# Performance work log

Measured on AMD Instinct MI355X. Metric: run time of the kernel, lower is better.

The kernel has to match this reference:

```python
import jax, jax.numpy as jnp
import numpy as np
from jax import lax

STRIDE = 2
PADDING = 2
KERNEL = 5


def _conv_transpose3d(x, weight, bias):
    # weight: [C_in, C_out, kd, kh, kw] (PyTorch ConvTranspose3d layout)
    # Equivalent dense conv: flip kernel spatially, swap in/out channels,
    # lhs_dilation=stride, symmetric padding = dilation*(k-1) - padding.
    w_t = jnp.flip(weight, axis=(2, 3, 4)).transpose(1, 0, 2, 3, 4)  # [C_out, C_in, k,k,k]
    pad = KERNEL - 1 - PADDING  # = 2
    y = lax.conv_general_dilated(
        x, w_t,
        window_strides=(1, 1, 1),
        padding=[(pad, pad)] * 3,
        lhs_dilation=(STRIDE, STRIDE, STRIDE),
        dimension_numbers=("NCDHW", "OIDHW", "NCDHW"),
    )
    return y + bias[None, :, None, None, None]


def _maxpool3d(y, k):
    # PyTorch MaxPool3d(kernel=k) -> stride=k, no padding, floor mode == VALID
    win = (1, 1, k, k, k)
    return lax.reduce_window(y, -jnp.inf, lax.max, win, win, "VALID")


def setup_inputs() -> dict:
    key = jax.random.key(0)
    k1, k2, k3 = jax.random.split(key, 3)
    x = jax.random.normal(k1, (16, 32, 16, 32, 32), dtype=jnp.float32)
    weight = jax.random.normal(k2, (32, 64, 5, 5, 5), dtype=jnp.float32) * 0.05
    bias = jax.random.normal(k3, (64,), dtype=jnp.float32) * 0.05
    return {"x": x, "weight": weight, "bias": bias}


def reference(x, weight, bias):
    y = _conv_transpose3d(x, weight, bias)     # [16, 64, 31, 63, 63]
    y = _maxpool3d(y, 2)                       # [16, 64, 15, 31, 31]
    y = _maxpool3d(y, 3)                       # [16, 64, 5, 10, 10]
    return jnp.sum(y, axis=1, keepdims=True)   # [16, 1, 5, 10, 10]
```

## Files before the change

kernel.cpp:

```cpp
#include <hip/hip_runtime.h>
#include <hip/hip_bf16.h>
#include <math.h>

typedef short bf16x8 __attribute__((ext_vector_type(8)));
typedef float f32x4 __attribute__((ext_vector_type(4)));

constexpr int CIN = 32, COUT = 64, D = 16, H = 32, W = 32;

constexpr size_t WS_XT_OFF = 1u << 20;
constexpr size_t WS_NEED   = WS_XT_OFF + 33554432u;

static __device__ const unsigned char IT_CODE[24] = {
    0, 8, 16, 3,
    1, 9, 17, 11, 19, 7,
    2, 10, 18, 5, 13, 21, 15,
    4, 12, 20, 6, 14, 22, 23};
static __device__ const unsigned char IT_START[5] = {0, 4, 10, 17, 24};
static __device__ const unsigned char EPI_START[10] = {0, 1, 3, 5, 6, 7, 9, 11, 12, 13};
static __device__ const unsigned char EPI_CNT[10]   = {1, 2, 2, 1, 1, 2, 2, 1, 1, 2};

__global__ void prep_all(const float* __restrict__ x, const float* __restrict__ w,
                         unsigned short* __restrict__ xT, unsigned short* __restrict__ wtp) {
    __shared__ float tile[32 * 33];
    int tid = threadIdx.x;
    if (blockIdx.x < 8192) {
        int bid = blockIdx.x;
        int ih = bid & 31, id = (bid >> 5) & 15, n = bid >> 9;
        int lw = tid & 31, g = tid >> 5;
#pragma unroll
        for (int p = 0; p < 4; ++p) {
            int ci = g + p * 8;
            tile[lw * 33 + ci] = x[((((size_t)n * CIN + ci) * D + id) * H + ih) * W + lw];
        }
        __syncthreads();
        unsigned short* op = xT + ((((size_t)n * D + id) * H + ih) * W) * CIN;
#pragma unroll
        for (int p = 0; p < 4; ++p) {
            int iw = g + p * 8;
            __hip_bfloat16 b = __float2bfloat16(tile[iw * 33 + lw]);
            op[iw * 32 + lw] = *reinterpret_cast<unsigned short*>(&b);
        }
    } else {
        int idx = (blockIdx.x - 8192) * 256 + tid;
        int ci  = idx & 31;
        int co  = (idx >> 5) & 63;
        int tt  = idx >> 11;
        int t   = tt % 27, cls = tt / 27;
        int td = t / 9, th = (t / 3) % 3, tw = t % 3;
        int pd = (cls >> 2) & 1, ph = (cls >> 1) & 1, pw = cls & 1;
        int kd = pd + 2 * td, kh = ph + 2 * th, kw = pw + 2 * tw;
        float v = 0.f;
        if (kd < 5 && kh < 5 && kw < 5)
            v = w[(ci * COUT + co) * 125 + kd * 25 + kh * 5 + kw];
        __hip_bfloat16 b = __float2bfloat16(v);
        wtp[idx] = *reinterpret_cast<unsigned short*>(&b);
    }
}

__global__ __launch_bounds__(256, 2) void main_k(
    const unsigned short* __restrict__ wtp, const unsigned short* __restrict__ xT,
    const float* __restrict__ bias, float* __restrict__ out)
{
    __shared__ unsigned short Xs[25600];
    int bx = blockIdx.x;
    int h0 = bx % 10;
    int d0 = (bx / 10) % 5;
    int n  = bx / 50;
    int tid = threadIdx.x;

    int id0 = 3 * d0 - 1, ih0 = 3 * h0 - 1;
    for (int i = tid; i < 3200; i += 256) {
        int cb = i & 3, ww = (i >> 2) & 31, hl = (i >> 7) % 5, dd = i / 640;
        int id = id0 + dd, ih = ih0 + hl, iw = ww - 1;
        float4 v = {0.f, 0.f, 0.f, 0.f};
        if (id >= 0 && ih >= 0 && iw >= 0)
            v = ((const float4*)(xT + ((((size_t)n * D + id) * H + ih) * W + iw) * 32))[cb];
        ((float4*)Xs)[i] = v;
    }

    int lane = tid & 63, wv = tid >> 6;
    int l15 = lane & 15, quad = lane >> 4;
    int wv_s = __builtin_amdgcn_readfirstlane(wv);

    int loff0 = l15 * 64 + quad * 16;
    int m1 = 16 + l15; if (m1 > 29) m1 = 29;
    int loff1 = m1 * 64 + quad * 16;
    int laneB = l15 * 64 + quad * 16;

    f32x4 mx[2][4];
#pragma unroll
    for (int mt = 0; mt < 2; ++mt)
#pragma unroll
        for (int nt = 0; nt < 4; ++nt) mx[mt][nt] = (f32x4){-INFINITY, -INFINITY, -INFINITY, -INFINITY};

    __syncthreads();
    const char* xsb = (const char*)Xs;

    int it0 = IT_START[wv_s], it1 = IT_START[wv_s + 1];
#pragma unroll 1
    for (int ii = it0; ii < it1; ++ii) {
        int code  = __builtin_amdgcn_readfirstlane(IT_CODE[ii]);
        int cls   = code & 7;
        int alpha = code >> 3;
        int ntd = 3 - ((cls >> 2) & 1), nth = 3 - ((cls >> 1) & 1), ntw = 3 - (cls & 1);
        const char* tbb = (const char*)wtp + (size_t)cls * 27 * 4096 + laneB;

        f32x4 acc[3][2][4];
#pragma unroll
        for (int b = 0; b < 3; ++b)
#pragma unroll
            for (int mt = 0; mt < 2; ++mt)
#pragma unroll
                for (int nt = 0; nt < 4; ++nt) acc[b][mt][nt] = (f32x4){0.f, 0.f, 0.f, 0.f};

        const int T = ntd * nth * ntw;
        bf16x8 nb0 = *(const bf16x8*)(tbb);
        bf16x8 nb1 = *(const bf16x8*)(tbb + 1024);
        bf16x8 nb2 = *(const bf16x8*)(tbb + 2048);
        bf16x8 nb3 = *(const bf16x8*)(tbb + 3072);
        int ptd = 0, pth = 0, ptw = 0;
        int nS = ((alpha + 2) * 5 + 2) * 2048 + 2 * 64;

#pragma unroll 1
        for (int it = 0; it < T; ++it) {
            bf16x8 b0 = nb0, b1 = nb1, b2 = nb2, b3 = nb3;
            const int S = nS;

            if (it + 1 < T) {
                ++ptw;
                if (ptw == ntw) { ptw = 0; ++pth; if (pth == nth) { pth = 0; ++ptd; } }
            }
            nS = ((alpha + 2 - ptd) * 5 + (2 - pth)) * 2048 + (2 - ptw) * 64;
            const char* bq = tbb + (ptd * 9 + pth * 3 + ptw) * 4096;
            nb0 = *(const bf16x8*)(bq);
            nb1 = *(const bf16x8*)(bq + 1024);
            nb2 = *(const bf16x8*)(bq + 2048);
            nb3 = *(const bf16x8*)(bq + 3072);

#pragma unroll
            for (int beta = 0; beta < 3; ++beta) {
                const char* rb = xsb + S + beta * 2048;
                bf16x8 af0 = *(const bf16x8*)(rb + loff0);
                bf16x8 af1 = *(const bf16x8*)(rb + loff1);
                acc[beta][0][0] = __builtin_amdgcn_mfma_f32_16x16x32_bf16(af0, b0, acc[beta][0][0], 0, 0, 0);
                acc[beta][0][1] = __builtin_amdgcn_mfma_f32_16x16x32_bf16(af0, b1, acc[beta][0][1], 0, 0, 0);
                acc[beta][0][2] = __builtin_amdgcn_mfma_f32_16x16x32_bf16(af0, b2, acc[beta][0][2], 0, 0, 0);
                acc[beta][0][3] = __builtin_amdgcn_mfma_f32_16x16x32_bf16(af0, b3, acc[beta][0][3], 0, 0, 0);
                acc[beta][1][0] = __builtin_amdgcn_mfma_f32_16x16x32_bf16(af1, b0, acc[beta][1][0], 0, 0, 0);
                acc[beta][1][1] = __builtin_amdgcn_mfma_f32_16x16x32_bf16(af1, b1, acc[beta][1][1], 0, 0, 0);
                acc[beta][1][2] = __builtin_amdgcn_mfma_f32_16x16x32_bf16(af1, b2, acc[beta][1][2], 0, 0, 0);
                acc[beta][1][3] = __builtin_amdgcn_mfma_f32_16x16x32_bf16(af1, b3, acc[beta][1][3], 0, 0, 0);
            }
        }

#pragma unroll
        for (int mt = 0; mt < 2; ++mt)
#pragma unroll
            for (int nt = 0; nt < 4; ++nt)
#pragma unroll
                for (int r = 0; r < 4; ++r) {
                    float m = fmaxf(fmaxf(acc[0][mt][nt][r], acc[1][mt][nt][r]), acc[2][mt][nt][r]);
                    mx[mt][nt][r] = fmaxf(mx[mt][nt][r], m);
                }
    }

    __syncthreads();
    float* epi = (float*)Xs;
    int fsm0 = (0x3123 >> (quad * 4)) & 15;
    int fsm1 = (0x4312 >> (quad * 4)) & 15;
#pragma unroll
    for (int mt = 0; mt < 2; ++mt) {
        int fs = mt ? fsm1 : fsm0;
        int g  = mt * 4 + quad;
#pragma unroll
        for (int nt = 0; nt < 4; ++nt) {
            float a0 = mx[mt][nt][0], a1 = mx[mt][nt][1], a2 = mx[mt][nt][2], a3 = mx[mt][nt][3];
            float t01 = fmaxf(a0, a1), t012 = fmaxf(t01, a2), t0123 = fmaxf(t012, a3);
            float pA = fs == 1 ? a0 : (fs == 2 ? t01 : (fs == 3 ? t012 : t0123));
            float t23 = fmaxf(a2, a3), t123 = fmaxf(a1, t23);
            float pB = fs == 1 ? t123 : (fs == 2 ? t23 : (fs == 3 ? a3 : -INFINITY));
            epi[((wv * 8 + g) * 2 + 0) * 64 + nt * 16 + l15] = pA;
            epi[((wv * 8 + g) * 2 + 1) * 64 + nt * 16 + l15] = pB;
        }
    }
    __syncthreads();

    int elemBase = ((n * 5 + d0) * 10 + h0) * 10;
    float bco = bias[lane];
#pragma unroll 1
    for (int win = wv_s; win < 10; win += 4) {
        int st = EPI_START[win], cnt = EPI_CNT[win];
        float v = -INFINITY;
        for (int src = 0; src < 4; ++src)
            for (int e = st; e < st + cnt; ++e)
                v = fmaxf(v, epi[(src * 16 + e) * 64 + lane]);
        v += bco;
#pragma unroll
        for (int off = 32; off > 0; off >>= 1) v += __shfl_xor(v, off);
        if (lane == 0) out[elemBase + win] = v;
    }
}

__global__ __launch_bounds__(256) void fused_fallback(
    const float* __restrict__ x, const float* __restrict__ wsrc,
    const float* __restrict__ bias, float* __restrict__ out)
{
    __shared__ float xs[CIN * 125];
    __shared__ float wmax[4][64];
    const int b  = blockIdx.x;
    const int w0 = b % 10, h0 = (b / 10) % 10, d0 = (b / 100) % 5, n = b / 500;
    const int tid = threadIdx.x;
    const int id0 = 3 * d0 - 1, ih0 = 3 * h0 - 1, iw0 = 3 * w0 - 1;
    for (int e = tid; e < CIN * 125; e += 256) {
        int kk = e % 5, jj = (e / 5) % 5, ii = (e / 25) % 5, c = e / 125;
        int id = id0 + ii, ih = ih0 + jj, iw = iw0 + kk;
        float v = 0.f;
        if (id >= 0 && ih >= 0 && iw >= 0)
            v = x[(((n * CIN + c) * D + id) * H + ih) * W + iw];
        xs[e] = v;
    }
    __syncthreads();
    const int lane = tid & 63, wv = tid >> 6;
    float lmax = -INFINITY;
    for (int ccls = 0; ccls < 2; ++ccls) {
        const int cls = wv * 2 + ccls;
        const int pd = (cls >> 2) & 1, ph = (cls >> 1) & 1, pw = cls & 1;
        float acc[27];
#pragma unroll
        for (int i = 0; i < 27; ++i) acc[i] = 0.f;
        for (int ci = 0; ci < CIN; ++ci) {
            float wr[27];
#pragma unroll
            for (int t = 0; t < 27; ++t) {
                int td = t / 9, th = (t / 3) % 3, tw = t % 3;
                int kd = pd + 2 * td, kh = ph + 2 * th, kw = pw + 2 * tw;
                wr[t] = (kd < 5 && kh < 5 && kw < 5)
                          ? wsrc[((ci * 64 + lane) * 125) + kd * 25 + kh * 5 + kw] : 0.f;
            }
            const float* xb = xs + ci * 125;
#pragma unroll
            for (int td = 0; td < 3; ++td)
#pragma unroll
            for (int th = 0; th < 3; ++th)
#pragma unroll
            for (int tw = 0; tw < 3; ++tw) {
                const float wval = wr[(td * 3 + th) * 3 + tw];
#pragma unroll
                for (int a = 0; a < 3; ++a)
#pragma unroll
                for (int bb = 0; bb < 3; ++bb)
#pragma unroll
                for (int cc = 0; cc < 3; ++cc)
                    acc[(a * 3 + bb) * 3 + cc] +=
                        xb[(a + 2 - td) * 25 + (bb + 2 - th) * 5 + (cc + 2 - tw)] * wval;
            }
        }
#pragma unroll
        for (int i = 0; i < 27; ++i) lmax = fmaxf(lmax, acc[i]);
    }
    wmax[wv][lane] = lmax;
    __syncthreads();
    if (wv == 0) {
        float m = fmaxf(fmaxf(wmax[0][lane], wmax[1][lane]),
                        fmaxf(wmax[2][lane], wmax[3][lane]));
        m += bias[lane];
        for (int off = 32; off > 0; off >>= 1) m += __shfl_down(m, off);
        if (lane == 0) out[b] = m;
    }
}

extern "C" void kernel_launch(void* const* d_in, const int* in_sizes, int n_in,
                              void* d_out, int out_size, void* d_ws, size_t ws_size,
                              hipStream_t stream) {
    const float* x    = (const float*)d_in[0];
    const float* w    = (const float*)d_in[1];
    const float* bias = (const float*)d_in[2];
    float* out = (float*)d_out;

    if (ws_size >= WS_NEED) {
        unsigned short* wtp = (unsigned short*)d_ws;
        unsigned short* xT  = (unsigned short*)((char*)d_ws + WS_XT_OFF);
        prep_all<<<9920, 256, 0, stream>>>(x, w, xT, wtp);
        main_k<<<800, 256, 0, stream>>>(wtp, xT, bias, out);
    } else {
        fused_fallback<<<8000, 256, 0, stream>>>(x, w, bias, out);
    }
}
```

Before: 206.2 us.

## Swizzle LDS input tile, vectorize prep transpose, raise main kernel occupancy

```diff
diff --git a/kernel.cpp b/kernel.cpp
--- a/kernel.cpp
+++ b/kernel.cpp
@@ -19,29 +19,37 @@
 static __device__ const unsigned char EPI_START[10] = {0, 1, 3, 5, 6, 7, 9, 11, 12, 13};
 static __device__ const unsigned char EPI_CNT[10]   = {1, 2, 2, 1, 1, 2, 2, 1, 1, 2};
 
-__global__ void prep_all(const float* __restrict__ x, const float* __restrict__ w,
-                         unsigned short* __restrict__ xT, unsigned short* __restrict__ wtp) {
-    __shared__ float tile[32 * 33];
+__global__ __launch_bounds__(1024) void prep_all(
+    const float* __restrict__ x, const float* __restrict__ w,
+    unsigned short* __restrict__ xT, unsigned short* __restrict__ wtp) {
+    __shared__ float tile[4][32][33];
     int tid = threadIdx.x;
-    if (blockIdx.x < 8192) {
-        int bid = blockIdx.x;
-        int ih = bid & 31, id = (bid >> 5) & 15, n = bid >> 9;
-        int lw = tid & 31, g = tid >> 5;
-#pragma unroll
-        for (int p = 0; p < 4; ++p) {
-            int ci = g + p * 8;
-            tile[lw * 33 + ci] = x[((((size_t)n * CIN + ci) * D + id) * H + ih) * W + lw];
+    if (blockIdx.x < 2048) {
+        int sub = tid >> 8, t = tid & 255;
+        int tileIdx = blockIdx.x * 4 + sub;
+        int ih = tileIdx & 31, id = (tileIdx >> 5) & 15, n = tileIdx >> 9;
+        int ci = t >> 3, iwq = t & 7;
+        float4 v = ((const float4*)(x + ((((size_t)n * CIN + ci) * D + id) * H + ih) * W))[iwq];
+        tile[sub][ci][iwq * 4 + 0] = v.x;
+        tile[sub][ci][iwq * 4 + 1] = v.y;
+        tile[sub][ci][iwq * 4 + 2] = v.z;
+        tile[sub][ci][iwq * 4 + 3] = v.w;
+        __syncthreads();
+        int iw = t >> 3, ciq = t & 7;
+        ushort4 o;
+        {
+            __hip_bfloat16 b0 = __float2bfloat16(tile[sub][ciq * 4 + 0][iw]);
+            __hip_bfloat16 b1 = __float2bfloat16(tile[sub][ciq * 4 + 1][iw]);
+            __hip_bfloat16 b2 = __float2bfloat16(tile[sub][ciq * 4 + 2][iw]);
+            __hip_bfloat16 b3 = __float2bfloat16(tile[sub][ciq * 4 + 3][iw]);
+            o.x = *reinterpret_cast<unsigned short*>(&b0);
+            o.y = *reinterpret_cast<unsigned short*>(&b1);
+            o.z = *reinterpret_cast<unsigned short*>(&b2);
+            o.w = *reinterpret_cast<unsigned short*>(&b3);
         }
-        __syncthreads();
-        unsigned short* op = xT + ((((size_t)n * D + id) * H + ih) * W) * CIN;
-#pragma unroll
-        for (int p = 0; p < 4; ++p) {
-            int iw = g + p * 8;
-            __hip_bfloat16 b = __float2bfloat16(tile[iw * 33 + lw]);
-            op[iw * 32 + lw] = *reinterpret_cast<unsigned short*>(&b);
-        }
+        ((ushort4*)(xT + ((((size_t)n * D + id) * H + ih) * W) * 32))[iw * 8 + ciq] = o;
     } else {
-        int idx = (blockIdx.x - 8192) * 256 + tid;
+        int idx = (blockIdx.x - 2048) * 1024 + tid;
         int ci  = idx & 31;
         int co  = (idx >> 5) & 63;
         int tt  = idx >> 11;
@@ -57,7 +65,11 @@
     }
 }
 
-__global__ __launch_bounds__(256, 2) void main_k(
+__device__ __forceinline__ int lpA(int wrow, int quad) {
+    return wrow * 64 + ((quad ^ ((wrow >> 1) & 3)) << 4);
+}
+
+__global__ __launch_bounds__(256, 3) void main_k(
     const unsigned short* __restrict__ wtp, const unsigned short* __restrict__ xT,
     const float* __restrict__ bias, float* __restrict__ out)
 {
@@ -75,17 +87,17 @@
         float4 v = {0.f, 0.f, 0.f, 0.f};
         if (id >= 0 && ih >= 0 && iw >= 0)
             v = ((const float4*)(xT + ((((size_t)n * D + id) * H + ih) * W + iw) * 32))[cb];
-        ((float4*)Xs)[i] = v;
+        ((float4*)Xs)[(i >> 2) * 4 + (cb ^ ((ww >> 1) & 3))] = v;
     }
 
     int lane = tid & 63, wv = tid >> 6;
     int l15 = lane & 15, quad = lane >> 4;
     int wv_s = __builtin_amdgcn_readfirstlane(wv);
 
-    int loff0 = l15 * 64 + quad * 16;
+    int laneB = l15 * 64 + quad * 16;
     int m1 = 16 + l15; if (m1 > 29) m1 = 29;
-    int loff1 = m1 * 64 + quad * 16;
-    int laneB = l15 * 64 + quad * 16;
+    int lp00 = lpA(l15 + 0, quad), lp01 = lpA(l15 + 1, quad), lp02 = lpA(l15 + 2, quad);
+    int lp10 = lpA(m1 + 0, quad),  lp11 = lpA(m1 + 1, quad),  lp12 = lpA(m1 + 2, quad);
 
     f32x4 mx[2][4];
 #pragma unroll
@@ -119,29 +131,34 @@
         bf16x8 nb2 = *(const bf16x8*)(tbb + 2048);
         bf16x8 nb3 = *(const bf16x8*)(tbb + 3072);
         int ptd = 0, pth = 0, ptw = 0;
-        int nS = ((alpha + 2) * 5 + 2) * 2048 + 2 * 64;
+        int nQb = ((alpha + 2) * 5 + 2) * 2048;
+        int nss = 2;
 
 #pragma unroll 1
         for (int it = 0; it < T; ++it) {
             bf16x8 b0 = nb0, b1 = nb1, b2 = nb2, b3 = nb3;
-            const int S = nS;
+            const int Qb = nQb, ss = nss;
 
             if (it + 1 < T) {
                 ++ptw;
                 if (ptw == ntw) { ptw = 0; ++pth; if (pth == nth) { pth = 0; ++ptd; } }
             }
-            nS = ((alpha + 2 - ptd) * 5 + (2 - pth)) * 2048 + (2 - ptw) * 64;
+            nQb = ((alpha + 2 - ptd) * 5 + (2 - pth)) * 2048;
+            nss = 2 - ptw;
             const char* bq = tbb + (ptd * 9 + pth * 3 + ptw) * 4096;
             nb0 = *(const bf16x8*)(bq);
             nb1 = *(const bf16x8*)(bq + 1024);
             nb2 = *(const bf16x8*)(bq + 2048);
             nb3 = *(const bf16x8*)(bq + 3072);
 
+            int lpa = ss == 0 ? lp00 : (ss == 1 ? lp01 : lp02);
+            int lpb = ss == 0 ? lp10 : (ss == 1 ? lp11 : lp12);
+
 #pragma unroll
             for (int beta = 0; beta < 3; ++beta) {
-                const char* rb = xsb + S + beta * 2048;
-                bf16x8 af0 = *(const bf16x8*)(rb + loff0);
-                bf16x8 af1 = *(const bf16x8*)(rb + loff1);
+                const char* rb = xsb + Qb + beta * 2048;
+                bf16x8 af0 = *(const bf16x8*)(rb + lpa);
+                bf16x8 af1 = *(const bf16x8*)(rb + lpb);
                 acc[beta][0][0] = __builtin_amdgcn_mfma_f32_16x16x32_bf16(af0, b0, acc[beta][0][0], 0, 0, 0);
                 acc[beta][0][1] = __builtin_amdgcn_mfma_f32_16x16x32_bf16(af0, b1, acc[beta][0][1], 0, 0, 0);
                 acc[beta][0][2] = __builtin_amdgcn_mfma_f32_16x16x32_bf16(af0, b2, acc[beta][0][2], 0, 0, 0);
@@ -280,7 +297,7 @@
     if (ws_size >= WS_NEED) {
         unsigned short* wtp = (unsigned short*)d_ws;
         unsigned short* xT  = (unsigned short*)((char*)d_ws + WS_XT_OFF);
-        prep_all<<<9920, 256, 0, stream>>>(x, w, xT, wtp);
+        prep_all<<<2480, 1024, 0, stream>>>(x, w, xT, wtp);
         main_k<<<800, 256, 0, stream>>>(wtp, xT, bias, out);
     } else {
         fused_fallback<<<8000, 256, 0, stream>>>(x, w, bias, out);
```

Result: slower. 212.9 us (+3.3%).

## Fuse input transpose/bf16 cast into main kernel with swizzled LDS layout

Applied to the files above, without the earlier changes.

```diff
diff --git a/kernel.cpp b/kernel.cpp
--- a/kernel.cpp
+++ b/kernel.cpp
@@ -7,8 +7,7 @@
 
 constexpr int CIN = 32, COUT = 64, D = 16, H = 32, W = 32;
 
-constexpr size_t WS_XT_OFF = 1u << 20;
-constexpr size_t WS_NEED   = WS_XT_OFF + 33554432u;
+constexpr size_t WS_NEED = 884736u;
 
 static __device__ const unsigned char IT_CODE[24] = {
     0, 8, 16, 3,
@@ -19,46 +18,28 @@
 static __device__ const unsigned char EPI_START[10] = {0, 1, 3, 5, 6, 7, 9, 11, 12, 13};
 static __device__ const unsigned char EPI_CNT[10]   = {1, 2, 2, 1, 1, 2, 2, 1, 1, 2};
 
-__global__ void prep_all(const float* __restrict__ x, const float* __restrict__ w,
-                         unsigned short* __restrict__ xT, unsigned short* __restrict__ wtp) {
-    __shared__ float tile[32 * 33];
-    int tid = threadIdx.x;
-    if (blockIdx.x < 8192) {
-        int bid = blockIdx.x;
-        int ih = bid & 31, id = (bid >> 5) & 15, n = bid >> 9;
-        int lw = tid & 31, g = tid >> 5;
-#pragma unroll
-        for (int p = 0; p < 4; ++p) {
-            int ci = g + p * 8;
-            tile[lw * 33 + ci] = x[((((size_t)n * CIN + ci) * D + id) * H + ih) * W + lw];
-        }
-        __syncthreads();
-        unsigned short* op = xT + ((((size_t)n * D + id) * H + ih) * W) * CIN;
-#pragma unroll
-        for (int p = 0; p < 4; ++p) {
-            int iw = g + p * 8;
-            __hip_bfloat16 b = __float2bfloat16(tile[iw * 33 + lw]);
-            op[iw * 32 + lw] = *reinterpret_cast<unsigned short*>(&b);
-        }
-    } else {
-        int idx = (blockIdx.x - 8192) * 256 + tid;
-        int ci  = idx & 31;
-        int co  = (idx >> 5) & 63;
-        int tt  = idx >> 11;
-        int t   = tt % 27, cls = tt / 27;
-        int td = t / 9, th = (t / 3) % 3, tw = t % 3;
-        int pd = (cls >> 2) & 1, ph = (cls >> 1) & 1, pw = cls & 1;
-        int kd = pd + 2 * td, kh = ph + 2 * th, kw = pw + 2 * tw;
-        float v = 0.f;
-        if (kd < 5 && kh < 5 && kw < 5)
-            v = w[(ci * COUT + co) * 125 + kd * 25 + kh * 5 + kw];
-        __hip_bfloat16 b = __float2bfloat16(v);
-        wtp[idx] = *reinterpret_cast<unsigned short*>(&b);
-    }
+__global__ void prep_w(const float* __restrict__ w, unsigned short* __restrict__ wtp) {
+    int idx = blockIdx.x * 256 + threadIdx.x;
+    int ci  = idx & 31;
+    int co  = (idx >> 5) & 63;
+    int tt  = idx >> 11;
+    int t   = tt % 27, cls = tt / 27;
+    int td = t / 9, th = (t / 3) % 3, tw = t % 3;
+    int pd = (cls >> 2) & 1, ph = (cls >> 1) & 1, pw = cls & 1;
+    int kd = pd + 2 * td, kh = ph + 2 * th, kw = pw + 2 * tw;
+    float v = 0.f;
+    if (kd < 5 && kh < 5 && kw < 5)
+        v = w[(ci * COUT + co) * 125 + kd * 25 + kh * 5 + kw];
+    __hip_bfloat16 b = __float2bfloat16(v);
+    wtp[idx] = *reinterpret_cast<unsigned short*>(&b);
+}
+
+__device__ __forceinline__ int lpA(int wrow, int quad) {
+    return wrow * 64 + ((quad ^ ((wrow >> 1) & 3)) << 4);
 }
 
 __global__ __launch_bounds__(256, 2) void main_k(
-    const unsigned short* __restrict__ wtp, const unsigned short* __restrict__ xT,
+    const unsigned short* __restrict__ wtp, const float* __restrict__ x,
     const float* __restrict__ bias, float* __restrict__ out)
 {
     __shared__ unsigned short Xs[25600];
@@ -69,23 +50,42 @@
     int tid = threadIdx.x;
 
     int id0 = 3 * d0 - 1, ih0 = 3 * h0 - 1;
-    for (int i = tid; i < 3200; i += 256) {
-        int cb = i & 3, ww = (i >> 2) & 31, hl = (i >> 7) % 5, dd = i / 640;
-        int id = id0 + dd, ih = ih0 + hl, iw = ww - 1;
+    for (int u = tid; u < 6400; u += 256) {
+        int q  = u & 7;
+        int ci = (u >> 3) & 31;
+        int p  = u >> 8;
+        int dd = p / 5, hl = p % 5;
+        int id = id0 + dd, ih = ih0 + hl;
         float4 v = {0.f, 0.f, 0.f, 0.f};
-        if (id >= 0 && ih >= 0 && iw >= 0)
-            v = ((const float4*)(xT + ((((size_t)n * D + id) * H + ih) * W + iw) * 32))[cb];
-        ((float4*)Xs)[i] = v;
+        if (id >= 0 && ih >= 0)
+            v = ((const float4*)(x + (((size_t)(n * CIN + ci) * D + id) * H + ih) * W))[q];
+        unsigned short hj[4];
+        {
+            __hip_bfloat16 b0 = __float2bfloat16(v.x); hj[0] = *reinterpret_cast<unsigned short*>(&b0);
+            __hip_bfloat16 b1 = __float2bfloat16(v.y); hj[1] = *reinterpret_cast<unsigned short*>(&b1);
+            __hip_bfloat16 b2 = __float2bfloat16(v.z); hj[2] = *reinterpret_cast<unsigned short*>(&b2);
+            __hip_bfloat16 b3 = __float2bfloat16(v.w); hj[3] = *reinterpret_cast<unsigned short*>(&b3);
+        }
+        int rowb = p * 1024;
+        int cig = ci >> 3, cil = ci & 7;
+#pragma unroll
+        for (int j = 0; j < 4; ++j) {
+            int ww = 4 * q + 1 + j;
+            if (ww < 32)
+                Xs[rowb + ww * 32 + ((cig ^ ((ww >> 1) & 3)) << 3) + cil] = hj[j];
+        }
+        if (q == 0)
+            Xs[rowb + (cig << 3) + cil] = 0;
     }
 
     int lane = tid & 63, wv = tid >> 6;
     int l15 = lane & 15, quad = lane >> 4;
     int wv_s = __builtin_amdgcn_readfirstlane(wv);
 
-    int loff0 = l15 * 64 + quad * 16;
+    int laneB = l15 * 64 + quad * 16;
     int m1 = 16 + l15; if (m1 > 29) m1 = 29;
-    int loff1 = m1 * 64 + quad * 16;
-    int laneB = l15 * 64 + quad * 16;
+    int lp00 = lpA(l15 + 0, quad), lp01 = lpA(l15 + 1, quad), lp02 = lpA(l15 + 2, quad);
+    int lp10 = lpA(m1 + 0, quad),  lp11 = lpA(m1 + 1, quad),  lp12 = lpA(m1 + 2, quad);
 
     f32x4 mx[2][4];
 #pragma unroll
@@ -104,6 +104,7 @@
         int alpha = code >> 3;
         int ntd = 3 - ((cls >> 2) & 1), nth = 3 - ((cls >> 1) & 1), ntw = 3 - (cls & 1);
         const char* tbb = (const char*)wtp + (size_t)cls * 27 * 4096 + laneB;
+        const int T = ntd * nth * ntw;
 
         f32x4 acc[3][2][4];
 #pragma unroll
@@ -113,43 +114,85 @@
 #pragma unroll
                 for (int nt = 0; nt < 4; ++nt) acc[b][mt][nt] = (f32x4){0.f, 0.f, 0.f, 0.f};
 
-        const int T = ntd * nth * ntw;
-        bf16x8 nb0 = *(const bf16x8*)(tbb);
-        bf16x8 nb1 = *(const bf16x8*)(tbb + 1024);
-        bf16x8 nb2 = *(const bf16x8*)(tbb + 2048);
-        bf16x8 nb3 = *(const bf16x8*)(tbb + 3072);
         int ptd = 0, pth = 0, ptw = 0;
-        int nS = ((alpha + 2) * 5 + 2) * 2048 + 2 * 64;
+        auto adv = [&]() {
+            ++ptw;
+            if (ptw == ntw) { ptw = 0; ++pth; if (pth == nth) { pth = 0; ++ptd; } }
+        };
+
+        int Qb_e = ((alpha + 2) * 5 + 2) * 2048, ss_e = 2;
+        bf16x8 bE0 = *(const bf16x8*)(tbb);
+        bf16x8 bE1 = *(const bf16x8*)(tbb + 1024);
+        bf16x8 bE2 = *(const bf16x8*)(tbb + 2048);
+        bf16x8 bE3 = *(const bf16x8*)(tbb + 3072);
+        adv();
+        int Qb_o = ((alpha + 2 - ptd) * 5 + (2 - pth)) * 2048, ss_o = 2 - ptw;
+        const char* bqo = tbb + (ptd * 9 + pth * 3 + ptw) * 4096;
+        bf16x8 bO0 = *(const bf16x8*)(bqo);
+        bf16x8 bO1 = *(const bf16x8*)(bqo + 1024);
+        bf16x8 bO2 = *(const bf16x8*)(bqo + 2048);
+        bf16x8 bO3 = *(const bf16x8*)(bqo + 3072);
+        adv();
 
 #pragma unroll 1
-        for (int it = 0; it < T; ++it) {
-            bf16x8 b0 = nb0, b1 = nb1, b2 = nb2, b3 = nb3;
-            const int S = nS;
-
+        for (int it = 0; it < T; it += 2) {
+            {
+                int lpa = ss_e == 0 ? lp00 : (ss_e == 1 ? lp01 : lp02);
+                int lpb = ss_e == 0 ? lp10 : (ss_e == 1 ? lp11 : lp12);
+#pragma unroll
+                for (int beta = 0; beta < 3; ++beta) {
+                    const char* rb = xsb + Qb_e + beta * 2048;
+                    bf16x8 af0 = *(const bf16x8*)(rb + lpa);
+                    bf16x8 af1 = *(const bf16x8*)(rb + lpb);
+                    acc[beta][0][0] = __builtin_amdgcn_mfma_f32_16x16x32_bf16(af0, bE0, acc[beta][0][0], 0, 0, 0);
+                    acc[beta][0][1] = __builtin_amdgcn_mfma_f32_16x16x32_bf16(af0, bE1, acc[beta][0][1], 0, 0, 0);
+                    acc[beta][0][2] = __builtin_amdgcn_mfma_f32_16x16x32_bf16(af0, bE2, acc[beta][0][2], 0, 0, 0);
+                    acc[beta][0][3] = __builtin_amdgcn_mfma_f32_16x16x32_bf16(af0, bE3, acc[beta][0][3], 0, 0, 0);
+                    acc[beta][1][0] = __builtin_amdgcn_mfma_f32_16x16x32_bf16(af1, bE0, acc[beta][1][0], 0, 0, 0);
+                    acc[beta][1][1] = __builtin_amdgcn_mfma_f32_16x16x32_bf16(af1, bE1, acc[beta][1][1], 0, 0, 0);
+                    acc[beta][1][2] = __builtin_amdgcn_mfma_f32_16x16x32_bf16(af1, bE2, acc[beta][1][2], 0, 0, 0);
+                    acc[beta][1][3] = __builtin_amdgcn_mfma_f32_16x16x32_bf16(af1, bE3, acc[beta][1][3], 0, 0, 0);
+                }
+            }
+            if (it + 2 < T) {
+                const char* bq = tbb + (ptd * 9 + pth * 3 + ptw) * 4096;
+                Qb_e = ((alpha + 2 - ptd) * 5 + (2 - pth)) * 2048;
+                ss_e = 2 - ptw;
+                bE0 = *(const bf16x8*)(bq);
+                bE1 = *(const bf16x8*)(bq + 1024);
+                bE2 = *(const bf16x8*)(bq + 2048);
+                bE3 = *(const bf16x8*)(bq + 3072);
+                adv();
+            }
             if (it + 1 < T) {
-                ++ptw;
-                if (ptw == ntw) { ptw = 0; ++pth; if (pth == nth) { pth = 0; ++ptd; } }
-            }
-            nS = ((alpha + 2 - ptd) * 5 + (2 - pth)) * 2048 + (2 - ptw) * 64;
-            const char* bq = tbb + (ptd * 9 + pth * 3 + ptw) * 4096;
-            nb0 = *(const bf16x8*)(bq);
-            nb1 = *(const bf16x8*)(bq + 1024);
-            nb2 = *(const bf16x8*)(bq + 2048);
-            nb3 = *(const bf16x8*)(bq + 3072);
-
-#pragma unroll
-            for (int beta = 0; beta < 3; ++beta) {
-                const char* rb = xsb + S + beta * 2048;
-                bf16x8 af0 = *(const bf16x8*)(rb + loff0);
-                bf16x8 af1 = *(const bf16x8*)(rb + loff1);
-                acc[beta][0][0] = __builtin_amdgcn_mfma_f32_16x16x32_bf16(af0, b0, acc[beta][0][0], 0, 0, 0);
-                acc[beta][0][1] = __builtin_amdgcn_mfma_f32_16x16x32_bf16(af0, b1, acc[beta][0][1], 0, 0, 0);
-                acc[beta][0][2] = __builtin_amdgcn_mfma_f32_16x16x32_bf16(af0, b2, acc[beta][0][2], 0, 0, 0);
-                acc[beta][0][3] = __builtin_amdgcn_mfma_f32_16x16x32_bf16(af0, b3, acc[beta][0][3], 0, 0, 0);
-                acc[beta][1][0] = __builtin_amdgcn_mfma_f32_16x16x32_bf16(af1, b0, acc[beta][1][0], 0, 0, 0);
-                acc[beta][1][1] = __builtin_amdgcn_mfma_f32_16x16x32_bf16(af1, b1, acc[beta][1][1], 0, 0, 0);
-                acc[beta][1][2] = __builtin_amdgcn_mfma_f32_16x16x32_bf16(af1, b2, acc[beta][1][2], 0, 0, 0);
-                acc[beta][1][3] = __builtin_amdgcn_mfma_f32_16x16x32_bf16(af1, b3, acc[beta][1][3], 0, 0, 0);
+                {
+                    int lpa = ss_o == 0 ? lp00 : (ss_o == 1 ? lp01 : lp02);
+                    int lpb = ss_o == 0 ? lp10 : (ss_o == 1 ? lp11 : lp12);
+#pragma unroll
+                    for (int beta = 0; beta < 3; ++beta) {
+                        const char* rb = xsb + Qb_o + beta * 2048;
+                        bf16x8 af0 = *(const bf16x8*)(rb + lpa);
+                        bf16x8 af1 = *(const bf16x8*)(rb + lpb);
+                        acc[beta][0][0] = __builtin_amdgcn_mfma_f32_16x16x32_bf16(af0, bO0, acc[beta][0][0], 0, 0, 0);
+                        acc[beta][0][1] = __builtin_amdgcn_mfma_f32_16x16x32_bf16(af0, bO1, acc[beta][0][1], 0, 0, 0);
+                        acc[beta][0][2] = __builtin_amdgcn_mfma_f32_16x16x32_bf16(af0, bO2, acc[beta][0][2], 0, 0, 0);
+                        acc[beta][0][3] = __builtin_amdgcn_mfma_f32_16x16x32_bf16(af0, bO3, acc[beta][0][3], 0, 0, 0);
+                        acc[beta][1][0] = __builtin_amdgcn_mfma_f32_16x16x32_bf16(af1, bO0, acc[beta][1][0], 0, 0, 0);
+                        acc[beta][1][1] = __builtin_amdgcn_mfma_f32_16x16x32_bf16(af1, bO1, acc[beta][1][1], 0, 0, 0);
+                        acc[beta][1][2] = __builtin_amdgcn_mfma_f32_16x16x32_bf16(af1, bO2, acc[beta][1][2], 0, 0, 0);
+                        acc[beta][1][3] = __builtin_amdgcn_mfma_f32_16x16x32_bf16(af1, bO3, acc[beta][1][3], 0, 0, 0);
+                    }
+                }
+                if (it + 3 < T) {
+                    const char* bq = tbb + (ptd * 9 + pth * 3 + ptw) * 4096;
+                    Qb_o = ((alpha + 2 - ptd) * 5 + (2 - pth)) * 2048;
+                    ss_o = 2 - ptw;
+                    bO0 = *(const bf16x8*)(bq);
+                    bO1 = *(const bf16x8*)(bq + 1024);
+                    bO2 = *(const bf16x8*)(bq + 2048);
+                    bO3 = *(const bf16x8*)(bq + 3072);
+                    adv();
+                }
             }
         }
 
@@ -279,9 +322,8 @@
 
     if (ws_size >= WS_NEED) {
         unsigned short* wtp = (unsigned short*)d_ws;
-        unsigned short* xT  = (unsigned short*)((char*)d_ws + WS_XT_OFF);
-        prep_all<<<9920, 256, 0, stream>>>(x, w, xT, wtp);
-        main_k<<<800, 256, 0, stream>>>(wtp, xT, bias, out);
+        prep_w<<<1728, 256, 0, stream>>>(w, wtp);
+        main_k<<<800, 256, 0, stream>>>(wtp, x, bias, out);
     } else {
         fused_fallback<<<8000, 256, 0, stream>>>(x, w, bias, out);
     }
```

After: 206.1 us. No clear change (-0.0%).
